# Kernel tuning notes

Measured on AMD Instinct MI355X. Metric: run time of the kernel, lower is better.

Reference implementation:

```python
import jax, jax.numpy as jnp
import numpy as np

B, N, F_DIM, R_DIM = 4, 512, 64, 128


def _pair_indices(n):
    # Same order as the original python double loop: i outer, j inner, skip i==j.
    ii, jj = np.meshgrid(np.arange(n), np.arange(n), indexing='ij')
    mask = ii != jj
    return jnp.asarray(ii[mask]), jnp.asarray(jj[mask])  # each [N*(N-1)]


def setup_inputs() -> dict:
    key = jax.random.key(0)
    ks = jax.random.split(key, 7)
    s1 = 1.0 / np.sqrt(2 * F_DIM)
    s2 = 1.0 / np.sqrt(R_DIM)
    return {
        'features': jax.random.normal(ks[0], (B, N, F_DIM), dtype=jnp.float32),
        'W1': jax.random.uniform(ks[1], (2 * F_DIM, R_DIM), jnp.float32, -s1, s1),
        'b1': jax.random.uniform(ks[2], (R_DIM,), jnp.float32, -s1, s1),
        'W2': jax.random.uniform(ks[3], (R_DIM, R_DIM), jnp.float32, -s2, s2),
        'b2': jax.random.uniform(ks[4], (R_DIM,), jnp.float32, -s2, s2),
        'W3': jax.random.uniform(ks[5], (R_DIM, 1), jnp.float32, -s2, s2),
        'b3': jax.random.uniform(ks[6], (1,), jnp.float32, -s2, s2),
    }


def reference(features, W1, b1, W2, b2, W3, b3):
    n = features.shape[1]
    idx_i, idx_j = _pair_indices(n)
    # Gather all ordered pairs (i != j): [B, P, 2F]
    pair = jnp.concatenate([features[:, idx_i, :], features[:, idx_j, :]], axis=-1)
    h = jax.nn.relu(jnp.einsum('bpf,fr->bpr', pair, W1) + b1)
    h = jax.nn.relu(jnp.einsum('bpr,rs->bps', h, W2) + b2)
    out = jnp.einsum('bpr,ro->bpo', h, W3) + b3  # [B, P, 1]
    return out
```

## Files before the change

### kernel.cpp

```cpp
#include <hip/hip_runtime.h>
#include <stdint.h>

#define B_ 4
#define N_ 512
#define F_ 64
#define R_ 128
#define PPI 511
#define TJ 128

typedef _Float16 f16x8 __attribute__((ext_vector_type(8)));
typedef _Float16 f16x2 __attribute__((ext_vector_type(2)));
typedef float f32x4 __attribute__((ext_vector_type(4)));

__device__ __forceinline__ uint16_t f16bits(float x) {
  return __builtin_bit_cast(uint16_t, (_Float16)x);
}
__device__ __forceinline__ f16x2 cvt_pk(float a, float b) {
  return __builtin_bit_cast(f16x2, __builtin_amdgcn_cvt_pkrtz(a, b));
}

__global__ __launch_bounds__(256) void prep_all(
    const float* __restrict__ feat, const float* __restrict__ W1,
    const float* __restrict__ b1, const float* __restrict__ W2,
    uint16_t* __restrict__ U, uint16_t* __restrict__ V, uint16_t* __restrict__ w2f) {
  if (blockIdx.x >= 1024) {
    const int d = (blockIdx.x - 1024) * 256 + threadIdx.x;
    const int jj = d & 7, lane = (d >> 3) & 63, tc = d >> 9;
    const int c = tc & 3, t = tc >> 2;
    const int rr = 32 * c + (lane >> 4) * 8 + jj;
    const int s = 16 * t + (lane & 15);
    w2f[d] = f16bits(W2[rr * R_ + s]);
    return;
  }
  __shared__ float fs[2][F_];
  const int row0 = blockIdx.x * 2;
  const int tid = threadIdx.x;
  if (tid < 2 * F_) fs[tid >> 6][tid & 63] = feat[row0 * F_ + tid];
  __syncthreads();
  const int r = tid & 127, rh = tid >> 7;
  const int row = row0 + rh;
  float u0 = b1[r], u1 = 0.f, v0 = 0.f, v1 = 0.f;
#pragma unroll
  for (int f = 0; f < F_; f += 2) {
    const float x0 = fs[rh][f], x1 = fs[rh][f + 1];
    u0 = fmaf(x0, W1[f * R_ + r], u0);
    v0 = fmaf(x0, W1[(F_ + f) * R_ + r], v0);
    u1 = fmaf(x1, W1[(f + 1) * R_ + r], u1);
    v1 = fmaf(x1, W1[(F_ + f + 1) * R_ + r], v1);
  }
  U[row * R_ + r] = f16bits(u0 + u1);
  V[row * R_ + r] = f16bits(v0 + v1);
}

__global__ __launch_bounds__(256, 3) void relnet_main(
    const uint16_t* __restrict__ U, const uint16_t* __restrict__ V,
    const uint16_t* __restrict__ w2f, const float* __restrict__ b2,
    const float* __restrict__ W3, const float* __restrict__ b3,
    float* __restrict__ out) {
  __shared__ __align__(16) uint16_t Vs[TJ * 128];

  const int bid = blockIdx.x;
  const int jb = bid & 3, ib = (bid >> 2) & 255, b = bid >> 10;
  const int i0 = ib * 2, j0 = jb * TJ;
  const int tid = threadIdx.x;

  {
    const uint4* sv = (const uint4*)(V + (b * N_ + j0) * R_);
    for (int l = tid; l < TJ * 16; l += 256) {
      const int row = l >> 4, seg = l & 15;
      const int col = (seg * 16) ^ ((row & 7) << 4);
      *(uint4*)((char*)Vs + row * 256 + col) = sv[row * 16 + seg];
    }
  }

  const int lane = tid & 63, wave = tid >> 6;
  const int quad = lane >> 4, l4 = lane & 15;
  const int il = wave >> 1, th = wave & 1;
  const int i = i0 + il;

  f16x8 w2r[4][4];
#pragma unroll
  for (int tp = 0; tp < 4; ++tp)
#pragma unroll
    for (int c = 0; c < 4; ++c) {
      const int t = th * 4 + tp;
      const uint4 w = *(const uint4*)(w2f + ((size_t)((t * 4 + c) * 64 + lane)) * 8);
      w2r[tp][c] = __builtin_bit_cast(f16x8, w);
    }

  f32x4 b2f[4];
  f16x2 w3p[4][2];
#pragma unroll
  for (int tp = 0; tp < 4; ++tp) {
    const int s0 = 16 * (th * 4 + tp) + 4 * quad;
    b2f[tp] = (f32x4){b2[s0], b2[s0 + 1], b2[s0 + 2], b2[s0 + 3]};
    w3p[tp][0] = (f16x2){(_Float16)W3[s0], (_Float16)W3[s0 + 1]};
    w3p[tp][1] = (f16x2){(_Float16)W3[s0 + 2], (_Float16)W3[s0 + 3]};
  }

  f16x8 uf[4];
#pragma unroll
  for (int c = 0; c < 4; ++c)
    uf[c] = __builtin_bit_cast(f16x8,
        *(const uint4*)(U + (size_t)(b * N_ + i) * R_ + c * 32 + quad * 8));

  const f16x8 z8 = {};
  const f16x2 z2 = {};

  __syncthreads();

  float res[8];

#pragma unroll
  for (int jt = 0; jt < 8; ++jt) {
    f16x8 hb[4];
#pragma unroll
    for (int c = 0; c < 4; ++c) {
      const uint4 v = *(const uint4*)((const char*)Vs + (jt * 16 + l4) * 256 +
                                      ((c * 64 + quad * 16) ^ ((l4 & 7) << 4)));
      hb[c] = __builtin_elementwise_max(__builtin_bit_cast(f16x8, v) + uf[c], z8);
    }

    f32x4 acc[4];
    __builtin_amdgcn_s_setprio(1);
#pragma unroll
    for (int tp = 0; tp < 4; ++tp)
      acc[tp] = __builtin_amdgcn_mfma_f32_16x16x32_f16(w2r[tp][0], hb[0], b2f[tp], 0, 0, 0);
#pragma unroll
    for (int c = 1; c < 4; ++c)
#pragma unroll
      for (int tp = 0; tp < 4; ++tp)
        acc[tp] = __builtin_amdgcn_mfma_f32_16x16x32_f16(w2r[tp][c], hb[c], acc[tp], 0, 0, 0);
    __builtin_amdgcn_s_setprio(0);

    float t0 = 0.f, t1 = 0.f, t2 = 0.f, t3 = 0.f;
#pragma unroll
    for (int tp = 0; tp < 4; tp += 2) {
      f16x2 p0 = __builtin_elementwise_max(cvt_pk(acc[tp][0], acc[tp][1]), z2);
      f16x2 p1 = __builtin_elementwise_max(cvt_pk(acc[tp][2], acc[tp][3]), z2);
      t0 = __builtin_amdgcn_fdot2(p0, w3p[tp][0], t0, false);
      t1 = __builtin_amdgcn_fdot2(p1, w3p[tp][1], t1, false);
      f16x2 q0 = __builtin_elementwise_max(cvt_pk(acc[tp + 1][0], acc[tp + 1][1]), z2);
      f16x2 q1 = __builtin_elementwise_max(cvt_pk(acc[tp + 1][2], acc[tp + 1][3]), z2);
      t2 = __builtin_amdgcn_fdot2(q0, w3p[tp + 1][0], t2, false);
      t3 = __builtin_amdgcn_fdot2(q1, w3p[tp + 1][1], t3, false);
    }
    res[jt] = (t0 + t1) + (t2 + t3);
  }

  __syncthreads();

  {
    float* pls = (float*)Vs;
    const int base = ((th * 2 + il) * 8) * 64 + quad * 16 + l4;
#pragma unroll
    for (int jt = 0; jt < 8; ++jt) pls[base + jt * 64] = res[jt];
  }

  __syncthreads();

  {
    const float* pls = (const float*)Vs;
    const int ril = tid >> 7, rjt = (tid >> 4) & 7, rl4 = tid & 15;
    float sum = b3[0];
#pragma unroll
    for (int h = 0; h < 2; ++h)
#pragma unroll
      for (int q = 0; q < 4; ++q)
        sum += pls[((h * 2 + ril) * 8 + rjt) * 64 + q * 16 + rl4];
    const int ri = i0 + ril;
    const int j = j0 + rjt * 16 + rl4;
    if (j != ri) {
      const int p = (b * N_ + ri) * PPI + (j < ri ? j : j - 1);
      out[p] = sum;
    }
  }
}

extern "C" void kernel_launch(void* const* d_in, const int* in_sizes, int n_in,
                              void* d_out, int out_size, void* d_ws, size_t ws_size,
                              hipStream_t stream) {
  const float* feat = (const float*)d_in[0];
  const float* W1 = (const float*)d_in[1];
  const float* b1 = (const float*)d_in[2];
  const float* W2 = (const float*)d_in[3];
  const float* b2 = (const float*)d_in[4];
  const float* W3 = (const float*)d_in[5];
  const float* b3 = (const float*)d_in[6];

  uint16_t* U = (uint16_t*)d_ws;
  uint16_t* V = U + (size_t)B_ * N_ * R_;
  uint16_t* w2f = V + (size_t)B_ * N_ * R_;

  prep_all<<<1024 + 64, 256, 0, stream>>>(feat, W1, b1, W2, U, V, w2f);
  relnet_main<<<B_ * (N_ / 2) * (N_ / TJ), 256, 0, stream>>>(U, V, w2f, b2, W3, b3,
                                                             (float*)d_out);
}
```

Before: 106.6 us.

## Loop over all j-blocks per workgroup with double-buffered LDS prefetch of V

```diff
diff --git a/kernel.cpp b/kernel.cpp
--- a/kernel.cpp
+++ b/kernel.cpp
@@ -52,27 +52,18 @@
   V[row * R_ + r] = f16bits(v0 + v1);
 }
 
-__global__ __launch_bounds__(256, 3) void relnet_main(
+__global__ __launch_bounds__(256, 2) void relnet_main(
     const uint16_t* __restrict__ U, const uint16_t* __restrict__ V,
     const uint16_t* __restrict__ w2f, const float* __restrict__ b2,
     const float* __restrict__ W3, const float* __restrict__ b3,
     float* __restrict__ out) {
-  __shared__ __align__(16) uint16_t Vs[TJ * 128];
+  __shared__ __align__(16) uint8_t smem[73728];
+  float* const pl = (float*)(smem + 65536);
 
   const int bid = blockIdx.x;
-  const int jb = bid & 3, ib = (bid >> 2) & 255, b = bid >> 10;
-  const int i0 = ib * 2, j0 = jb * TJ;
+  const int ib = bid & 255, b = bid >> 8;
+  const int i0 = ib * 2;
   const int tid = threadIdx.x;
-
-  {
-    const uint4* sv = (const uint4*)(V + (b * N_ + j0) * R_);
-    for (int l = tid; l < TJ * 16; l += 256) {
-      const int row = l >> 4, seg = l & 15;
-      const int col = (seg * 16) ^ ((row & 7) << 4);
-      *(uint4*)((char*)Vs + row * 256 + col) = sv[row * 16 + seg];
-    }
-  }
-
   const int lane = tid & 63, wave = tid >> 6;
   const int quad = lane >> 4, l4 = lane & 15;
   const int il = wave >> 1, th = wave & 1;
@@ -104,76 +95,98 @@
     uf[c] = __builtin_bit_cast(f16x8,
         *(const uint4*)(U + (size_t)(b * N_ + i) * R_ + c * 32 + quad * 8));
 
+  const float bias3 = b3[0];
   const f16x8 z8 = {};
   const f16x2 z2 = {};
 
+  const uint4* const Vb = (const uint4*)(V + (size_t)(b * N_) * R_);
+
+  uint4 st[8];
+#pragma unroll
+  for (int k = 0; k < 8; ++k) st[k] = Vb[tid + 256 * k];
+#pragma unroll
+  for (int k = 0; k < 8; ++k) {
+    const int l = tid + 256 * k, row = l >> 4, seg = l & 15;
+    *(uint4*)(smem + row * 256 + ((seg * 16) ^ ((row & 7) << 4))) = st[k];
+  }
   __syncthreads();
 
-  float res[8];
-
-#pragma unroll
-  for (int jt = 0; jt < 8; ++jt) {
-    f16x8 hb[4];
-#pragma unroll
-    for (int c = 0; c < 4; ++c) {
-      const uint4 v = *(const uint4*)((const char*)Vs + (jt * 16 + l4) * 256 +
-                                      ((c * 64 + quad * 16) ^ ((l4 & 7) << 4)));
-      hb[c] = __builtin_elementwise_max(__builtin_bit_cast(f16x8, v) + uf[c], z8);
-    }
-
-    f32x4 acc[4];
-    __builtin_amdgcn_s_setprio(1);
-#pragma unroll
-    for (int tp = 0; tp < 4; ++tp)
-      acc[tp] = __builtin_amdgcn_mfma_f32_16x16x32_f16(w2r[tp][0], hb[0], b2f[tp], 0, 0, 0);
-#pragma unroll
-    for (int c = 1; c < 4; ++c)
+  int curoff = 0;
+  for (int jb = 0; jb < 4; ++jb) {
+    if (jb < 3) {
+      const uint4* src = Vb + (size_t)(jb + 1) * TJ * (R_ / 8);
+#pragma unroll
+      for (int k = 0; k < 8; ++k) st[k] = src[tid + 256 * k];
+    }
+
+    const uint8_t* const buf = smem + curoff;
+
+#pragma unroll
+    for (int jt = 0; jt < 8; ++jt) {
+      f16x8 hb[4];
+#pragma unroll
+      for (int c = 0; c < 4; ++c) {
+        const uint4 v = *(const uint4*)(buf + (jt * 16 + l4) * 256 +
+                                        ((c * 64 + quad * 16) ^ ((l4 & 7) << 4)));
+        hb[c] = __builtin_elementwise_max(__builtin_bit_cast(f16x8, v) + uf[c], z8);
+      }
+
+      f32x4 acc[4];
+      __builtin_amdgcn_s_setprio(1);
 #pragma unroll
       for (int tp = 0; tp < 4; ++tp)
-        acc[tp] = __builtin_amdgcn_mfma_f32_16x16x32_f16(w2r[tp][c], hb[c], acc[tp], 0, 0, 0);
-    __builtin_amdgcn_s_setprio(0);
-
-    float t0 = 0.f, t1 = 0.f, t2 = 0.f, t3 = 0.f;
-#pragma unroll
-    for (int tp = 0; tp < 4; tp += 2) {
-      f16x2 p0 = __builtin_elementwise_max(cvt_pk(acc[tp][0], acc[tp][1]), z2);
-      f16x2 p1 = __builtin_elementwise_max(cvt_pk(acc[tp][2], acc[tp][3]), z2);
-      t0 = __builtin_amdgcn_fdot2(p0, w3p[tp][0], t0, false);
-      t1 = __builtin_amdgcn_fdot2(p1, w3p[tp][1], t1, false);
-      f16x2 q0 = __builtin_elementwise_max(cvt_pk(acc[tp + 1][0], acc[tp + 1][1]), z2);
-      f16x2 q1 = __builtin_elementwise_max(cvt_pk(acc[tp + 1][2], acc[tp + 1][3]), z2);
-      t2 = __builtin_amdgcn_fdot2(q0, w3p[tp + 1][0], t2, false);
-      t3 = __builtin_amdgcn_fdot2(q1, w3p[tp + 1][1], t3, false);
-    }
-    res[jt] = (t0 + t1) + (t2 + t3);
-  }
-
-  __syncthreads();
-
-  {
-    float* pls = (float*)Vs;
-    const int base = ((th * 2 + il) * 8) * 64 + quad * 16 + l4;
-#pragma unroll
-    for (int jt = 0; jt < 8; ++jt) pls[base + jt * 64] = res[jt];
-  }
-
-  __syncthreads();
-
-  {
-    const float* pls = (const float*)Vs;
-    const int ril = tid >> 7, rjt = (tid >> 4) & 7, rl4 = tid & 15;
-    float sum = b3[0];
-#pragma unroll
-    for (int h = 0; h < 2; ++h)
-#pragma unroll
-      for (int q = 0; q < 4; ++q)
-        sum += pls[((h * 2 + ril) * 8 + rjt) * 64 + q * 16 + rl4];
-    const int ri = i0 + ril;
-    const int j = j0 + rjt * 16 + rl4;
-    if (j != ri) {
-      const int p = (b * N_ + ri) * PPI + (j < ri ? j : j - 1);
-      out[p] = sum;
-    }
+        acc[tp] = __builtin_amdgcn_mfma_f32_16x16x32_f16(w2r[tp][0], hb[0], b2f[tp], 0, 0, 0);
+#pragma unroll
+      for (int c = 1; c < 4; ++c)
+#pragma unroll
+        for (int tp = 0; tp < 4; ++tp)
+          acc[tp] = __builtin_amdgcn_mfma_f32_16x16x32_f16(w2r[tp][c], hb[c], acc[tp], 0, 0, 0);
+      __builtin_amdgcn_s_setprio(0);
+
+      float t0 = 0.f, t1 = 0.f, t2 = 0.f, t3 = 0.f;
+#pragma unroll
+      for (int tp = 0; tp < 4; tp += 2) {
+        f16x2 p0 = __builtin_elementwise_max(cvt_pk(acc[tp][0], acc[tp][1]), z2);
+        f16x2 p1 = __builtin_elementwise_max(cvt_pk(acc[tp][2], acc[tp][3]), z2);
+        t0 = __builtin_amdgcn_fdot2(p0, w3p[tp][0], t0, false);
+        t1 = __builtin_amdgcn_fdot2(p1, w3p[tp][1], t1, false);
+        f16x2 q0 = __builtin_elementwise_max(cvt_pk(acc[tp + 1][0], acc[tp + 1][1]), z2);
+        f16x2 q1 = __builtin_elementwise_max(cvt_pk(acc[tp + 1][2], acc[tp + 1][3]), z2);
+        t2 = __builtin_amdgcn_fdot2(q0, w3p[tp + 1][0], t2, false);
+        t3 = __builtin_amdgcn_fdot2(q1, w3p[tp + 1][1], t3, false);
+      }
+      pl[(((th * 2 + il) * 8) + jt) * 64 + quad * 16 + l4] = (t0 + t1) + (t2 + t3);
+    }
+
+    if (jb < 3) {
+      uint8_t* const nbuf = smem + (curoff ^ 32768);
+#pragma unroll
+      for (int k = 0; k < 8; ++k) {
+        const int l = tid + 256 * k, row = l >> 4, seg = l & 15;
+        *(uint4*)(nbuf + row * 256 + ((seg * 16) ^ ((row & 7) << 4))) = st[k];
+      }
+    }
+
+    __syncthreads();
+
+    {
+      const int ril = tid >> 7, rjt = (tid >> 4) & 7, rl4 = tid & 15;
+      float sum = bias3;
+#pragma unroll
+      for (int h = 0; h < 2; ++h)
+#pragma unroll
+        for (int q = 0; q < 4; ++q)
+          sum += pl[((h * 2 + ril) * 8 + rjt) * 64 + q * 16 + rl4];
+      const int ri = i0 + ril;
+      const int j = jb * TJ + rjt * 16 + rl4;
+      if (j != ri) {
+        const int p = (b * N_ + ri) * PPI + (j < ri ? j : j - 1);
+        out[p] = sum;
+      }
+    }
+
+    __syncthreads();
+    curoff ^= 32768;
   }
 }
 
@@ -193,6 +206,6 @@
   uint16_t* w2f = V + (size_t)B_ * N_ * R_;
 
   prep_all<<<1024 + 64, 256, 0, stream>>>(feat, W1, b1, W2, U, V, w2f);
-  relnet_main<<<B_ * (N_ / 2) * (N_ / TJ), 256, 0, stream>>>(U, V, w2f, b2, W3, b3,
-                                                             (float*)d_out);
-}
+  relnet_main<<<B_ * (N_ / 2), 256, 0, stream>>>(U, V, w2f, b2, W3, b3,
+                                                 (float*)d_out);
+}
```

Result: slower. 125.2 us (+17.4%).
